# Optimization experiments

Measured on AMD Instinct MI355X. Metric: run time of the kernel, lower is better.

Reference implementation:

```python
import jax, jax.numpy as jnp
import numpy as np

N_NODES = 20000
N_EDGES = 300000
D = 256
NUM_RELS = 8
NUM_BASES = 4


def setup_inputs() -> dict:
    key = jax.random.key(0)
    ks = jax.random.split(key, 8)
    x = jax.random.normal(ks[0], (N_NODES, D), dtype=jnp.float32)
    src = jax.random.randint(ks[1], (N_EDGES,), 0, N_NODES, dtype=jnp.int32)
    dst = jax.random.randint(ks[2], (N_EDGES,), 0, N_NODES, dtype=jnp.int32)
    etypes = jax.random.randint(ks[3], (N_EDGES,), 0, NUM_RELS, dtype=jnp.int32)
    # basis-decomposition params (as in DGL RelGraphConv with regularizer='basis')
    scale = 1.0 / np.sqrt(D)
    basis = jax.random.normal(ks[4], (NUM_BASES, D, D), dtype=jnp.float32) * scale
    comp = jax.random.normal(ks[5], (NUM_RELS, NUM_BASES), dtype=jnp.float32)
    loop_weight = jax.random.normal(ks[6], (D, D), dtype=jnp.float32) * scale
    bias_param = jnp.zeros((D,), dtype=jnp.float32)
    return {"x": x, "src": src, "dst": dst, "etypes": etypes,
            "basis": basis, "comp": comp, "loop_weight": loop_weight,
            "bias_param": bias_param}


def reference(x, src, dst, etypes, basis, comp, loop_weight, bias_param):
    # Relation weights from basis decomposition: [R, D, D]
    W = jnp.einsum('rb,bio->rio', comp, basis)
    # Transform every node by every relation weight: [N, R, D]
    H = jnp.einsum('ni,rio->nro', x, W)
    # Per-edge message: gather source node's transform for the edge's relation: [E, D]
    msg = H[src, etypes]
    # Scatter-sum aggregation by destination node: [N, D]
    agg = jax.ops.segment_sum(msg, dst, num_segments=N_NODES)
    # Self-loop + bias (activation=None, dropout=0.0 in the wrapper's defaults)
    out = agg + x @ loop_weight + bias_param
    return out
```

## Files before the change

kernel.cpp:

```cpp
#include <hip/hip_runtime.h>

#define N_NODES 20000
#define N_EDGES 300000
#define DIM 256
#define NUM_RELS 8
#define NUM_BASES 4
#define NB 79
#define K2 1280
#define TROW 1024
#define PREPX_BLOCKS 2500
#define CAP 96
#define GBLK 2048

typedef float f32x4 __attribute__((ext_vector_type(4)));
typedef short s16x8 __attribute__((ext_vector_type(8)));

__device__ __forceinline__ unsigned short f2bf(float f) {
    unsigned u = __builtin_bit_cast(unsigned, f);
    u += 0x7fffu + ((u >> 16) & 1u);
    return (unsigned short)(u >> 16);
}
__device__ __forceinline__ float bf2f(unsigned short h) {
    unsigned u = ((unsigned)h) << 16;
    return __builtin_bit_cast(float, u);
}

__device__ __forceinline__ void gload_lds16(const void* g, void* l) {
    __builtin_amdgcn_global_load_lds((const __attribute__((address_space(1))) void*)g,
                                     (__attribute__((address_space(3))) void*)l,
                                     16, 0, 0);
}

__global__ __launch_bounds__(256) void prep_all(const float* __restrict__ x,
                                                const float* __restrict__ basis,
                                                const float* __restrict__ loopw,
                                                unsigned short* __restrict__ xb,
                                                unsigned short* __restrict__ W2,
                                                int* __restrict__ cnt) {
    int blk = blockIdx.x;
    if (blk < PREPX_BLOCKS) {
        int idx = (blk * 256 + threadIdx.x) * 8;
        float4 v0 = *reinterpret_cast<const float4*>(x + idx);
        float4 v1 = *reinterpret_cast<const float4*>(x + idx + 4);
        s16x8 o;
        o[0] = (short)f2bf(v0.x); o[1] = (short)f2bf(v0.y);
        o[2] = (short)f2bf(v0.z); o[3] = (short)f2bf(v0.w);
        o[4] = (short)f2bf(v1.x); o[5] = (short)f2bf(v1.y);
        o[6] = (short)f2bf(v1.z); o[7] = (short)f2bf(v1.w);
        *reinterpret_cast<s16x8*>(xb + idx) = o;
    } else if (blk < PREPX_BLOCKS + DIM) {
        int o = blk - PREPX_BLOCKS;
        int i = threadIdx.x;
#pragma unroll
        for (int b = 0; b < NUM_BASES; ++b)
            W2[(size_t)o * K2 + b * 256 + i] = f2bf(basis[((size_t)b * 256 + i) * 256 + o]);
        W2[(size_t)o * K2 + 1024 + i] = f2bf(loopw[(size_t)i * 256 + o]);
    } else {
        int i = (blk - PREPX_BLOCKS - DIM) * 256 + threadIdx.x;
        if (i < N_NODES) cnt[i] = 0;
    }
}

__global__ __launch_bounds__(256) void bucket_fill(const int* __restrict__ src,
                                                   const int* __restrict__ dst,
                                                   const int* __restrict__ et,
                                                   int* __restrict__ cnt,
                                                   int* __restrict__ bucket) {
    int e = blockIdx.x * 256 + threadIdx.x;
    if (e >= N_EDGES) return;
    int d = dst[e];
    int pos = atomicAdd(&cnt[d], 1);
    if (pos < CAP)
        bucket[(size_t)d * CAP + pos] = src[e] * NUM_RELS + et[e];
}

__device__ __forceinline__ void edge_fma(float acc[NUM_BASES][4],
                                         ushort4 v, float4 cw) {
    float x0 = bf2f(v.x), x1 = bf2f(v.y), x2 = bf2f(v.z), x3 = bf2f(v.w);
    acc[0][0] += cw.x * x0; acc[0][1] += cw.x * x1; acc[0][2] += cw.x * x2; acc[0][3] += cw.x * x3;
    acc[1][0] += cw.y * x0; acc[1][1] += cw.y * x1; acc[1][2] += cw.y * x2; acc[1][3] += cw.y * x3;
    acc[2][0] += cw.z * x0; acc[2][1] += cw.z * x1; acc[2][2] += cw.z * x2; acc[2][3] += cw.z * x3;
    acc[3][0] += cw.w * x0; acc[3][1] += cw.w * x1; acc[3][2] += cw.w * x2; acc[3][3] += cw.w * x3;
}

__global__ __launch_bounds__(256) void gather_T(const int* __restrict__ cnt,
                                                const int* __restrict__ bucket,
                                                const unsigned short* __restrict__ Xb,
                                                const float* __restrict__ comp,
                                                unsigned short* __restrict__ T) {
    const int wid0 = blockIdx.x * 4 + (threadIdx.x >> 6);
    const int lane = threadIdx.x & 63;
    const int c = lane * 4;
    const int wstride = GBLK * 4;

    for (int n = wid0; n < N_NODES; n += wstride) {
        float acc[NUM_BASES][4] = {};
        int deg = cnt[n]; if (deg > CAP) deg = CAP;
        const int base = n * CAP;

        int e = 0;
        for (; e + 7 < deg; e += 8) {
            int p[8];
#pragma unroll
            for (int i = 0; i < 8; ++i) p[i] = bucket[base + e + i];
            ushort4 v[8];
#pragma unroll
            for (int i = 0; i < 8; ++i)
                v[i] = *reinterpret_cast<const ushort4*>(Xb + (size_t)(p[i] >> 3) * DIM + c);
            float4 cw[8];
#pragma unroll
            for (int i = 0; i < 8; ++i)
                cw[i] = *reinterpret_cast<const float4*>(comp + (p[i] & 7) * 4);
#pragma unroll
            for (int i = 0; i < 8; ++i)
                edge_fma(acc, v[i], cw[i]);
        }
        for (; e + 3 < deg; e += 4) {
            int p[4];
#pragma unroll
            for (int i = 0; i < 4; ++i) p[i] = bucket[base + e + i];
            ushort4 v[4];
#pragma unroll
            for (int i = 0; i < 4; ++i)
                v[i] = *reinterpret_cast<const ushort4*>(Xb + (size_t)(p[i] >> 3) * DIM + c);
            float4 cw[4];
#pragma unroll
            for (int i = 0; i < 4; ++i)
                cw[i] = *reinterpret_cast<const float4*>(comp + (p[i] & 7) * 4);
#pragma unroll
            for (int i = 0; i < 4; ++i)
                edge_fma(acc, v[i], cw[i]);
        }
        for (; e < deg; ++e) {
            int p = bucket[base + e];
            ushort4 v = *reinterpret_cast<const ushort4*>(Xb + (size_t)(p >> 3) * DIM + c);
            float4 cw = *reinterpret_cast<const float4*>(comp + (p & 7) * 4);
            edge_fma(acc, v, cw);
        }

#pragma unroll
        for (int b = 0; b < NUM_BASES; ++b) {
            ushort4 o;
            o.x = f2bf(acc[b][0]); o.y = f2bf(acc[b][1]);
            o.z = f2bf(acc[b][2]); o.w = f2bf(acc[b][3]);
            *reinterpret_cast<ushort4*>(T + (size_t)n * TROW + b * 256 + c) = o;
        }
    }
}

#define BM 64
#define BN 256
#define BK 64
#define NT 20

__global__ __launch_bounds__(512) void gemm_out(const unsigned short* __restrict__ Tb,
                                                const unsigned short* __restrict__ Xb,
                                                const unsigned short* __restrict__ W2,
                                                const float* __restrict__ bias,
                                                float* __restrict__ out) {
    __shared__ unsigned short At[2][BM * BK];
    __shared__ unsigned short Bt[2][BN * BK];
    const int m0 = blockIdx.x * BM;
    const int t = threadIdx.x;
    const int lane = t & 63;
    const int w = t >> 6;
    const int wr = w >> 2;
    const int wc = w & 3;
    const int srow = lane >> 3;
    const int sgrp = lane & 7;

    f32x4 acc[2][4] = {};

    auto stage = [&](int kt, int b) {
        int k0 = kt * BK;
        const unsigned short* As; int astr, ac0;
        if (k0 < TROW) { As = Tb; astr = TROW; ac0 = k0; }
        else           { As = Xb; astr = DIM;  ac0 = k0 - TROW; }
        int scol = (sgrp ^ srow) << 3;
        {
            int rt = w * 8 + srow;
            int gr = m0 + rt; if (gr > N_NODES - 1) gr = N_NODES - 1;
            gload_lds16(As + (size_t)gr * astr + ac0 + scol, &At[b][(w * 8) * BK]);
        }
#pragma unroll
        for (int is = 0; is < 4; ++is) {
            int rt = w * 32 + is * 8 + srow;
            gload_lds16(W2 + (size_t)rt * K2 + k0 + scol, &Bt[b][(w * 32 + is * 8) * BK]);
        }
    };

    stage(0, 0);
    __syncthreads();

    for (int kt = 0; kt < NT; ++kt) {
        int cb = kt & 1;
        if (kt + 1 < NT) stage(kt + 1, cb ^ 1);
#pragma unroll
        for (int kk = 0; kk < BK; kk += 32) {
            const int gg = (kk >> 3) + (lane >> 4);
            s16x8 af[2], bfr[4];
#pragma unroll
            for (int m = 0; m < 2; ++m) {
                int r = wr * 32 + m * 16 + (lane & 15);
                af[m] = *reinterpret_cast<const s16x8*>(&At[cb][r * BK + ((gg ^ (r & 7)) << 3)]);
            }
#pragma unroll
            for (int n = 0; n < 4; ++n) {
                int r = wc * 64 + n * 16 + (lane & 15);
                bfr[n] = *reinterpret_cast<const s16x8*>(&Bt[cb][r * BK + ((gg ^ (r & 7)) << 3)]);
            }
#pragma unroll
            for (int m = 0; m < 2; ++m)
#pragma unroll
                for (int n = 0; n < 4; ++n)
                    acc[m][n] = __builtin_amdgcn_mfma_f32_16x16x32_bf16(af[m], bfr[n], acc[m][n], 0, 0, 0);
        }
        __syncthreads();
    }

    float b4[4];
#pragma unroll
    for (int n = 0; n < 4; ++n) b4[n] = bias[wc * 64 + n * 16 + (lane & 15)];
#pragma unroll
    for (int m = 0; m < 2; ++m) {
        int rbase = m0 + wr * 32 + m * 16 + ((lane >> 4) * 4);
#pragma unroll
        for (int j = 0; j < 4; ++j) {
            int row = rbase + j;
            if (row < N_NODES) {
#pragma unroll
                for (int n = 0; n < 4; ++n) {
                    int col = wc * 64 + n * 16 + (lane & 15);
                    out[(size_t)row * DIM + col] = acc[m][n][j] + b4[n];
                }
            }
        }
    }
}

extern "C" void kernel_launch(void* const* d_in, const int* in_sizes, int n_in,
                              void* d_out, int out_size, void* d_ws, size_t ws_size,
                              hipStream_t stream) {
    const float* x      = (const float*)d_in[0];
    const int*   src    = (const int*)d_in[1];
    const int*   dst    = (const int*)d_in[2];
    const int*   etypes = (const int*)d_in[3];
    const float* basis  = (const float*)d_in[4];
    const float* comp   = (const float*)d_in[5];
    const float* loopw  = (const float*)d_in[6];
    const float* bias   = (const float*)d_in[7];
    float* out = (float*)d_out;

    char* p = (char*)d_ws;
    unsigned short* W2 = (unsigned short*)p;            p += (size_t)DIM * K2 * 2;
    unsigned short* Xb = (unsigned short*)p;            p += (size_t)N_NODES * DIM * 2;
    unsigned short* T  = (unsigned short*)p;            p += (size_t)N_NODES * TROW * 2;
    int* cnt    = (int*)p;                              p += (size_t)N_NODES * 4;
    int* bucket = (int*)p;                              p += (size_t)N_NODES * CAP * 4;

    prep_all<<<PREPX_BLOCKS + DIM + NB, 256, 0, stream>>>(x, basis, loopw, Xb, W2, cnt);

    bucket_fill<<<(N_EDGES + 255) / 256, 256, 0, stream>>>(src, dst, etypes, cnt, bucket);

    gather_T<<<GBLK, 256, 0, stream>>>(cnt, bucket, Xb, comp, T);

    gemm_out<<<(N_NODES + BM - 1) / BM, 512, 0, stream>>>(T, Xb, W2, bias, out);
}
```

Measured before the change: 91.79 us.

## Split gather across edge groups and column quarters with shuffle reduction

```diff
diff --git a/kernel.cpp b/kernel.cpp
--- a/kernel.cpp
+++ b/kernel.cpp
@@ -10,7 +10,7 @@
 #define TROW 1024
 #define PREPX_BLOCKS 2500
 #define CAP 96
-#define GBLK 2048
+#define GQBLK 2048
 
 typedef float f32x4 __attribute__((ext_vector_type(4)));
 typedef short s16x8 __attribute__((ext_vector_type(8)));
@@ -90,60 +90,52 @@
                                                 unsigned short* __restrict__ T) {
     const int wid0 = blockIdx.x * 4 + (threadIdx.x >> 6);
     const int lane = threadIdx.x & 63;
-    const int c = lane * 4;
-    const int wstride = GBLK * 4;
-
-    for (int n = wid0; n < N_NODES; n += wstride) {
-        float acc[NUM_BASES][4] = {};
-        int deg = cnt[n]; if (deg > CAP) deg = CAP;
-        const int base = n * CAP;
-
-        int e = 0;
-        for (; e + 7 < deg; e += 8) {
-            int p[8];
-#pragma unroll
-            for (int i = 0; i < 8; ++i) p[i] = bucket[base + e + i];
-            ushort4 v[8];
-#pragma unroll
-            for (int i = 0; i < 8; ++i)
-                v[i] = *reinterpret_cast<const ushort4*>(Xb + (size_t)(p[i] >> 3) * DIM + c);
-            float4 cw[8];
-#pragma unroll
-            for (int i = 0; i < 8; ++i)
-                cw[i] = *reinterpret_cast<const float4*>(comp + (p[i] & 7) * 4);
-#pragma unroll
-            for (int i = 0; i < 8; ++i)
-                edge_fma(acc, v[i], cw[i]);
-        }
-        for (; e + 3 < deg; e += 4) {
-            int p[4];
-#pragma unroll
-            for (int i = 0; i < 4; ++i) p[i] = bucket[base + e + i];
-            ushort4 v[4];
-#pragma unroll
-            for (int i = 0; i < 4; ++i)
-                v[i] = *reinterpret_cast<const ushort4*>(Xb + (size_t)(p[i] >> 3) * DIM + c);
-            float4 cw[4];
-#pragma unroll
-            for (int i = 0; i < 4; ++i)
-                cw[i] = *reinterpret_cast<const float4*>(comp + (p[i] & 7) * 4);
-#pragma unroll
-            for (int i = 0; i < 4; ++i)
-                edge_fma(acc, v[i], cw[i]);
-        }
-        for (; e < deg; ++e) {
-            int p = bucket[base + e];
-            ushort4 v = *reinterpret_cast<const ushort4*>(Xb + (size_t)(p >> 3) * DIM + c);
-            float4 cw = *reinterpret_cast<const float4*>(comp + (p & 7) * 4);
-            edge_fma(acc, v, cw);
-        }
-
-#pragma unroll
-        for (int b = 0; b < NUM_BASES; ++b) {
-            ushort4 o;
-            o.x = f2bf(acc[b][0]); o.y = f2bf(acc[b][1]);
-            o.z = f2bf(acc[b][2]); o.w = f2bf(acc[b][3]);
-            *reinterpret_cast<ushort4*>(T + (size_t)n * TROW + b * 256 + c) = o;
+    const int g = lane >> 4;
+    const int cq = (lane & 15) * 4;
+    const int wstride = GQBLK * 4;
+
+    for (int q = 0; q < 4; ++q) {
+        const int cb = q * 64 + cq;
+        for (int n = wid0; n < N_NODES; n += wstride) {
+            int deg = cnt[n]; if (deg > CAP) deg = CAP;
+            const int base = n * CAP;
+            float acc[NUM_BASES][4] = {};
+
+            int e = g;
+            for (; e + 4 < deg; e += 8) {
+                int p0 = bucket[base + e];
+                int p1 = bucket[base + e + 4];
+                ushort4 v0 = *reinterpret_cast<const ushort4*>(Xb + (size_t)(p0 >> 3) * DIM + cb);
+                ushort4 v1 = *reinterpret_cast<const ushort4*>(Xb + (size_t)(p1 >> 3) * DIM + cb);
+                float4 c0 = *reinterpret_cast<const float4*>(comp + (p0 & 7) * 4);
+                float4 c1 = *reinterpret_cast<const float4*>(comp + (p1 & 7) * 4);
+                edge_fma(acc, v0, c0);
+                edge_fma(acc, v1, c1);
+            }
+            for (; e < deg; e += 4) {
+                int p = bucket[base + e];
+                ushort4 v = *reinterpret_cast<const ushort4*>(Xb + (size_t)(p >> 3) * DIM + cb);
+                float4 cw = *reinterpret_cast<const float4*>(comp + (p & 7) * 4);
+                edge_fma(acc, v, cw);
+            }
+
+#pragma unroll
+            for (int b = 0; b < NUM_BASES; ++b)
+#pragma unroll
+                for (int j = 0; j < 4; ++j) {
+                    acc[b][j] += __shfl_xor(acc[b][j], 16, 64);
+                    acc[b][j] += __shfl_xor(acc[b][j], 32, 64);
+                }
+
+            if (g == 0) {
+#pragma unroll
+                for (int b = 0; b < NUM_BASES; ++b) {
+                    ushort4 o;
+                    o.x = f2bf(acc[b][0]); o.y = f2bf(acc[b][1]);
+                    o.z = f2bf(acc[b][2]); o.w = f2bf(acc[b][3]);
+                    *reinterpret_cast<ushort4*>(T + (size_t)n * TROW + b * 256 + cb) = o;
+                }
+            }
         }
     }
 }
@@ -262,7 +254,7 @@
 
     bucket_fill<<<(N_EDGES + 255) / 256, 256, 0, stream>>>(src, dst, etypes, cnt, bucket);
 
-    gather_T<<<GBLK, 256, 0, stream>>>(cnt, bucket, Xb, comp, T);
+    gather_T<<<GQBLK, 256, 0, stream>>>(cnt, bucket, Xb, comp, T);
 
     gemm_out<<<(N_NODES + BM - 1) / BM, 512, 0, stream>>>(T, Xb, W2, bias, out);
 }
```

Result: slower. 105.6 us (+15.1%).
